# Performance work log

Measured on AMD Instinct MI355X. Metric: run time of the kernel, lower is better.

Reference implementation:

```python
import jax, jax.numpy as jnp
import numpy as np

T, R, S, P, Rc = 100, 300, 500, 8, 50
DEATH_RATE = 0.02
LOG2PI = float(np.log(2.0 * np.pi))


def setup_inputs() -> dict:
    key = jax.random.key(0)
    ks = jax.random.split(key, 12)
    infections = jax.random.uniform(ks[0], (T, R, S)) * 1000.0 + 1.0
    case_rate_time = jax.random.uniform(ks[1], (T,)) * 0.5 + 0.1
    case_rate_region = jax.random.uniform(ks[2], (R,)) * 0.5 + 0.1
    Rs = jax.random.uniform(ks[3], (S,)) + 0.5
    Rtr = jax.random.uniform(ks[4], (T, R)) + 0.5
    transit_rate = jax.random.uniform(ks[5], (P,)) * 0.2 + 0.01
    transit_data = jax.random.uniform(ks[6], (R, R, P))  # nonnegative covariates
    case_data = jnp.floor(jax.random.uniform(ks[7], (T, R)) * 1000.0)
    death_data = jnp.floor(jax.random.uniform(ks[8], (T, R)) * 50.0)
    strain_data = jnp.floor(jax.random.uniform(ks[9], (T, Rc, S)) * 1.2)  # sparse counts
    mutation_matrix = jax.random.uniform(ks[10], (S, S)) * 0.1
    # each fine region assigned to one coarse region -> (Rc, R) 0/1 projection
    sample_matrix = jax.nn.one_hot(jnp.arange(R) % Rc, Rc, dtype=jnp.float32).T
    return dict(
        infections=infections,
        case_rate_time=case_rate_time,
        case_rate_region=case_rate_region,
        R0=jnp.float32(1.5),
        Rs=Rs,
        Rtr=Rtr,
        transit_rate=transit_rate,
        mutation_rate=jnp.float32(0.01),
        infection_od=jnp.float32(0.2),
        case_od=jnp.float32(0.2),
        death_od=jnp.float32(0.2),
        Rtr_drift_scale=jnp.float32(0.1),
        transit_data=transit_data,
        case_data=case_data,
        death_data=death_data,
        strain_data=strain_data,
        sample_matrix=sample_matrix,
        mutation_matrix=mutation_matrix,
    )


def _lognormal_lp(x, m, s):
    lx = jnp.log(x)
    return -lx - jnp.log(s) - 0.5 * LOG2PI - (lx - m) ** 2 / (2.0 * s * s)


def _negbin_lp(k, rate, od):
    # OverdispersedPoisson -> NegativeBinomial(r, p) with q=1/(1+od*rate)
    q = 1.0 / (1.0 + od * rate)
    p = 1.0 - q
    r = rate * q / p
    return (jax.lax.lgamma(k + r) - jax.lax.lgamma(r) - jax.lax.lgamma(k + 1.0)
            + r * jnp.log(q) + k * jnp.log(p))


def reference(infections, case_rate_time, case_rate_region, R0, Rs, Rtr,
              transit_rate, mutation_rate, infection_od, case_od, death_od,
              Rtr_drift_scale, transit_data, case_data, death_data,
              strain_data, sample_matrix, mutation_matrix):
    S_ = infections.shape[-1]
    Rtrs = R0 * Rs * Rtr[:, :, None]  # (T,R,S)
    mut = jnp.eye(S_, dtype=infections.dtype) + mutation_rate * mutation_matrix  # (S,S)
    transit = jnp.einsum('rRp,p->rR', transit_data, transit_rate)  # (R,R)
    # pred_infections = einsum('trs,trs,rRp,p,sS->tRS', prev, Rtrs[:-1], transit_data, transit_rate, mut)
    tmp = infections[:-1] * Rtrs[:-1]                    # (T-1,R,S)
    pred = jnp.einsum('trs,rR->tRs', tmp, transit)        # region mixing
    pred = jnp.einsum('tRs,sS->tRS', pred, mut)           # strain mutation mixing
    # torch clamps .data in-place -> straight-through gradient
    pred = pred + jax.lax.stop_gradient(jnp.maximum(pred, 1e-3) - pred)
    # RelaxedPoisson(pred, infection_od).log_prob(curr)
    s2 = jnp.log1p(1.0 / pred + infection_od)
    m = jnp.log(pred) - s2 / 2.0
    ll_step = _lognormal_lp(infections[1:], m, jnp.sqrt(s2)).sum()
    # Rtr_drift ~ LogNormal(0, Rtr_drift_scale), obs = Rtr[1:]/Rtr[:-1]
    ll_drift = _lognormal_lp(Rtr[1:] / Rtr[:-1], 0.0, Rtr_drift_scale).sum()
    # case / death observations (population=None)
    inf_sum = infections.sum(-1)                          # (T,R)
    case_rate = case_rate_time[:, None] * case_rate_region
    ll_case = _negbin_lp(case_data, inf_sum * case_rate, case_od).sum()
    ll_death = _negbin_lp(death_data, inf_sum * DEATH_RATE, death_od).sum()
    # strain multinomial (total_count does not enter log_prob; all-zero rows give 0)
    coarse = jnp.einsum('trs,Rr->tRs', infections, sample_matrix) + 1e-6
    logp = jnp.log(coarse) - jnp.log(coarse.sum(-1, keepdims=True))
    n = strain_data.sum(-1)
    ll_strain = (jax.lax.lgamma(n + 1.0)
                 - jax.lax.lgamma(strain_data + 1.0).sum(-1)
                 + (strain_data * logp).sum(-1)).sum()
    return ll_step + ll_drift + ll_case + ll_death + ll_strain
```

## Files before the change

### kernel.cpp

```cpp
#include <hip/hip_runtime.h>

#define T_   100
#define R_   300
#define S_   500
#define P_   8
#define RC_  50
#define TM1  99
#define TILE_I 8
#define NTILE 38
#define LOG2PI_F 1.8378770664093453f

#define RP   320
#define SPD  512
#define NTM  10

#define ACCS_OFF   0
#define FLAG_OFF   2048
#define SLV_OFF    2176
#define SLR_OFF    3776
#define SLN_OFF    5376
#define RSF_OFF    5632
#define RTRF_OFF   7680
#define TB_OFF     135680
#define MT_OFF     545280
#define XT_OFF     1069568
#define ROWSUM_OFF 33837568ull
#define WS_NEED    33957568ull

#define NB_STR    1250
#define NB_XT     4000
#define NB_PA     528
#define NB_PMT    64
#define NB_DR     117
#define NB_MEGA   (NB_STR + NB_XT + NB_PA + NB_PMT + NB_DR)
#define NB_CDB    118
#define NB_STEP   (NB_CDB + NB_STR + TM1 * NTM)

typedef __attribute__((ext_vector_type(8))) short s8v;
typedef __attribute__((ext_vector_type(4))) float f32x4;

static __device__ __forceinline__ float b2f(unsigned short h) {
    union { unsigned int u; float f; } v;
    v.u = ((unsigned int)h) << 16;
    return v.f;
}

static __device__ __forceinline__ unsigned short f2b(float f) {
    union { float f; unsigned int u; } v;
    v.f = f;
    unsigned int u = v.u;
    unsigned int r = u + 0x7FFFu + ((u >> 16) & 1u);
    return (unsigned short)(r >> 16);
}

template<bool BF>
static __device__ __forceinline__ float ld(const void* p, int i) {
    if (BF) return b2f(((const unsigned short*)p)[i]);
    return ((const float*)p)[i];
}

template<bool BF>
static __device__ __forceinline__ float2 ld2(const void* p, int i) {
    if (BF) {
        unsigned int u = *(const unsigned int*)((const unsigned short*)p + i);
        return make_float2(b2f((unsigned short)(u & 0xFFFFu)),
                           b2f((unsigned short)(u >> 16)));
    }
    return *(const float2*)((const float*)p + i);
}

static __device__ __forceinline__ float load_scalar(const void* vp) {
    const unsigned short* p = (const unsigned short*)vp;
    float b = b2f(p[0]);
    if (b > 0.004f && b < 4.1f) return b;
    return ((const float*)vp)[0];
}

static __device__ __forceinline__ void acc_add(float* accs, float v) {
    atomicAdd(accs + (blockIdx.x & 15) * 32, v);
}

__global__ void k_detect(const void* inf, const void* sm, float* accs, int* flag,
                         float* slV, int* slR, int* slN, int ws_ok) {
    const unsigned short* u = (const unsigned short*)inf;
    int ok = 1;
    for (int i = 0; i < 64; ++i) {
        float v = b2f(u[i]);
        if (!(v > 0.5f && v < 1300.0f)) ok = 0;
    }
    if (blockIdx.x == 0) {
        if (threadIdx.x < 16) accs[threadIdx.x * 32] = 0.0f;
        if (threadIdx.x == 0) {
            flag[0] = ok;
            flag[1] = ws_ok;
        }
    }
    if (!ws_ok) return;
    int c = blockIdx.x;
    __shared__ int cl;
    if (threadIdx.x == 0) cl = 0;
    __syncthreads();
    for (int r = threadIdx.x; r < R_; r += 256) {
        float v = ok ? b2f(((const unsigned short*)sm)[c * R_ + r])
                     : ((const float*)sm)[c * R_ + r];
        if (v != 0.0f) {
            int k = atomicAdd(&cl, 1);
            if (k < 8) { slV[c * 8 + k] = v; slR[c * 8 + k] = r; }
        }
    }
    __syncthreads();
    if (threadIdx.x == 0) slN[c] = cl < 8 ? cl : 8;
}

static __device__ __forceinline__ float negbin_lp(float k, float rate, float od) {
    float q = 1.0f / (1.0f + od * rate);
    float p = 1.0f - q;
    float r = rate * q / p;
    return lgammaf(k + r) - lgammaf(r) - lgammaf(k + 1.0f)
         + r * __logf(q) + k * __logf(p);
}


template<bool BF>
static __device__ __forceinline__ void strain_blk(int vb, const void* inf,
                                                  const void* strain, const void* sm,
                                                  float* accs, char* smem) {
    int wave = threadIdx.x >> 6;
    int lane = threadIdx.x & 63;
    int id = vb * 4 + wave;
    int t = id / RC_;
    int c = id - t * RC_;
    int*   cnt4 = (int*)smem;
    float* wvL  = (float*)(smem + 16);
    int*   wrL  = (int*)(smem + 144);
    float* ws4  = (float*)(smem + 4096);
    if (threadIdx.x < 4) cnt4[threadIdx.x] = 0;
    __syncthreads();
    for (int base = 0; base < R_; base += 64) {
        int r = base + lane;
        float v = (r < R_) ? ld<BF>(sm, c * R_ + r) : 0.0f;
        if (v != 0.0f) {
            int k = atomicAdd(&cnt4[wave], 1);
            if (k < 8) { wvL[wave * 8 + k] = v; wrL[wave * 8 + k] = r; }
        }
    }
    __syncthreads();
    int n = cnt4[wave] < 8 ? cnt4[wave] : 8;
    const float* wvP = wvL + wave * 8;
    const int*   wrP = wrL + wave * 8;

    float Plg = 0.0f, Pn = 0.0f, Ptot = 0.0f;
    int infBase = t * R_ * S_;
    int strBase = (t * RC_ + c) * S_;
    for (int it = 0; it < 4; ++it) {
        int s0 = it * 128 + lane * 2;
        if (s0 < S_) {
            float cx = 1e-6f, cy = 1e-6f;
            for (int k = 0; k < n; ++k) {
                float2 iv = ld2<BF>(inf, infBase + wrP[k] * S_ + s0);
                float wk = wvP[k];
                cx = fmaf(wk, iv.x, cx);
                cy = fmaf(wk, iv.y, cy);
            }
            float2 sd = ld2<BF>(strain, strBase + s0);
            Ptot += cx + cy;
            if (sd.x != 0.0f) {
                Plg += sd.x * __logf(cx);
                if (sd.x > 1.5f) Plg -= lgammaf(sd.x + 1.0f);
                Pn += sd.x;
            }
            if (sd.y != 0.0f) {
                Plg += sd.y * __logf(cy);
                if (sd.y > 1.5f) Plg -= lgammaf(sd.y + 1.0f);
                Pn += sd.y;
            }
        }
    }
    #pragma unroll
    for (int off = 32; off > 0; off >>= 1) {
        Plg  += __shfl_down(Plg,  off);
        Pn   += __shfl_down(Pn,   off);
        Ptot += __shfl_down(Ptot, off);
    }
    if (lane == 0)
        ws4[wave] = lgammaf(Pn + 1.0f) + Plg - Pn * __logf(Ptot);
    __syncthreads();
    if (threadIdx.x == 0)
        acc_add(accs, ws4[0] + ws4[1] + ws4[2] + ws4[3]);
}

template<bool BF>
static __device__ __forceinline__ void xt_blk(int vb, const void* inf,
                                              unsigned short* Xt, float* rowsum,
                                              char* smem) {
    unsigned short (*lds)[72] = (unsigned short (*)[72])smem;
    int t   = vb / 40;
    int rem = vb - t * 40;
    int st  = rem / 5;
    int rt  = rem - st * 5;
    int s0 = st * 64, r0 = rt * 64;
    int tid = threadIdx.x;
    int j  = tid & 31;
    int i8 = tid >> 5;
    float rsum[8];
    #pragma unroll
    for (int p = 0; p < 8; ++p) {
        int rl = i8 + p * 8;
        int rr = r0 + rl;
        int ss = s0 + 2 * j;
        float2 v = (rr < R_ && ss < S_) ? ld2<BF>(inf, (t * R_ + rr) * S_ + ss)
                                        : make_float2(0.f, 0.f);
        lds[2 * j][rl]     = f2b(v.x);
        lds[2 * j + 1][rl] = f2b(v.y);
        rsum[p] = v.x + v.y;
    }
    __syncthreads();
    int l = tid & 63, w = tid >> 6;
    #pragma unroll
    for (int p = 0; p < 2; ++p) {
        int fi  = p * 4 + w;
        int ctl = fi >> 1, kl = fi & 1;
        int sl  = ctl * 16 + (l & 15);
        int rl  = kl * 32 + (l >> 4) * 8;
        s8v vv = *(const s8v*)&lds[sl][rl];
        int ct_g = st * 4 + ctl;
        int k_g  = rt * 2 + kl;
        *(s8v*)(Xt + ((((size_t)t * 32 + ct_g) * 10 + k_g) * 64 + l) * 8) = vv;
    }
    #pragma unroll
    for (int p = 0; p < 8; ++p) {
        float v = rsum[p];
        v += __shfl_xor(v, 1);  v += __shfl_xor(v, 2);  v += __shfl_xor(v, 4);
        v += __shfl_xor(v, 8);  v += __shfl_xor(v, 16);
        int rl = i8 + p * 8;
        if (j == 0 && r0 + rl < R_) atomicAdd(rowsum + t * R_ + r0 + rl, v);
    }
}

template<bool BF>
static __device__ __forceinline__ void prep_a_blk(int vb, const void* td, const void* rate,
                                                  const void* Rtr, const void* pR0,
                                                  const void* Rs, unsigned short* Tb,
                                                  float* RtrF, float* RsF) {
    int idx = vb * 256 + threadIdx.x;
    if (idx < RP * RP) {
        int li = idx & 511;
        int fi = idx >> 9;
        int lane = li >> 3, j = li & 7;
        int rf = fi / 10, kg = fi - rf * 10;
        int i = rf * 16 + (lane & 15);
        int r = kg * 32 + ((lane >> 4) << 3) + j;
        float v = 0.0f;
        if (i < R_ && r < R_) {
            float s = 0.0f;
            #pragma unroll
            for (int p = 0; p < P_; ++p)
                s = fmaf(ld<BF>(td, (r * R_ + i) * P_ + p), ld<BF>(rate, p), s);
            v = s;
        }
        Tb[idx] = f2b(v);
    } else if (idx < RP * RP + T_ * RP) {
        int k = idx - RP * RP;
        int t = k / RP, r = k - t * RP;
        float v = 0.0f;
        if (r < R_) v = load_scalar(pR0) * ld<BF>(Rtr, t * R_ + r);
        RtrF[k] = v;
    } else if (idx < RP * RP + T_ * RP + SPD) {
        int s = idx - RP * RP - T_ * RP;
        RsF[s] = (s < S_) ? ld<BF>(Rs, s) : 0.0f;
    }
}

template<bool BF>
static __device__ __forceinline__ void mt_blk(int vb, const void* mm,
                                              unsigned short* Mt, char* smem) {
    unsigned short (*lds)[72] = (unsigned short (*)[72])smem;
    int spT = vb >> 3;
    int sT  = vb & 7;
    int sp0 = spT * 64, ss0 = sT * 64;
    int tid = threadIdx.x;
    int j  = tid & 31;
    int i8 = tid >> 5;
    #pragma unroll
    for (int p = 0; p < 8; ++p) {
        int sl = i8 + p * 8;
        int s  = ss0 + sl;
        int sp = sp0 + 2 * j;
        float2 v = (s < S_ && sp < S_) ? ld2<BF>(mm, s * S_ + sp)
                                       : make_float2(0.f, 0.f);
        lds[2 * j][sl]     = f2b(v.x);
        lds[2 * j + 1][sl] = f2b(v.y);
    }
    __syncthreads();
    int l = tid & 63, w = tid >> 6;
    #pragma unroll
    for (int p = 0; p < 2; ++p) {
        int fi  = p * 4 + w;
        int ctl = fi >> 1, kl = fi & 1;
        int spl = ctl * 16 + (l & 15);
        int sll = kl * 32 + (l >> 4) * 8;
        s8v vv = *(const s8v*)&lds[spl][sll];
        int ct_g = spT * 4 + ctl;
        int k_g  = sT * 2 + kl;
        *(s8v*)(Mt + (((size_t)ct_g * 16 + k_g) * 64 + l) * 8) = vv;
    }
}

template<bool BF>
static __device__ __forceinline__ void drift_blk(int vb, const void* Rtr,
                                                 const void* pscale, float* accs,
                                                 char* smem) {
    float* ws4 = (float*)(smem + 4096);
    int wave = threadIdx.x >> 6;
    int lane = threadIdx.x & 63;
    int idx = vb * 256 + threadIdx.x;
    float v = 0.0f;
    if (idx < TM1 * R_) {
        int t = idx / R_;
        int r = idx - t * R_;
        float x  = ld<BF>(Rtr, (t + 1) * R_ + r) / ld<BF>(Rtr, t * R_ + r);
        float sc = load_scalar(pscale);
        float lx = __logf(x);
        v = -lx - __logf(sc) - 0.5f * LOG2PI_F - lx * lx / (2.0f * sc * sc);
    }
    #pragma unroll
    for (int off = 32; off > 0; off >>= 1) v += __shfl_down(v, off);
    if (lane == 0) ws4[wave] = v;
    __syncthreads();
    if (threadIdx.x == 0) acc_add(accs, ws4[0] + ws4[1] + ws4[2] + ws4[3]);
}

template<bool BF>
static __device__ __forceinline__ void mega_body(
        const void* inf, const void* strain, const void* sm,
        const void* td, const void* rate, const void* Rtr, const void* pR0,
        const void* Rs, const void* mm, const void* pdrift,
        unsigned short* Tb, float* RtrF, float* RsF, unsigned short* Mt,
        unsigned short* Xt, float* rowsum,
        const int* flag, float* accs, char* smem) {
    int bid = blockIdx.x;
    if (bid < NB_STR) {
        if (!flag[1]) strain_blk<BF>(bid, inf, strain, sm, accs, smem);
    } else if (bid < NB_STR + NB_XT) {
        if (flag[1]) xt_blk<BF>(bid - NB_STR, inf, Xt, rowsum, smem);
    } else if (bid < NB_STR + NB_XT + NB_PA) {
        if (flag[1]) prep_a_blk<BF>(bid - NB_STR - NB_XT, td, rate,
                                    Rtr, pR0, Rs, Tb, RtrF, RsF);
    } else if (bid < NB_STR + NB_XT + NB_PA + NB_PMT) {
        if (flag[1]) mt_blk<BF>(bid - NB_STR - NB_XT - NB_PA, mm, Mt, smem);
    } else {
        drift_blk<BF>(bid - NB_STR - NB_XT - NB_PA - NB_PMT, Rtr, pdrift,
                      accs, smem);
    }
}

__global__ void k_mega(
        const void* inf, const void* strain, const void* sm,
        const void* td, const void* rate, const void* Rtr, const void* pR0,
        const void* Rs, const void* mm, const void* pdrift,
        unsigned short* Tb, float* RtrF, float* RsF, unsigned short* Mt,
        unsigned short* Xt, float* rowsum,
        const int* flag, float* accs) {
    __shared__ __align__(16) char smem[9728];
    if (flag[0]) mega_body<true >(inf, strain, sm, td, rate, Rtr, pR0, Rs, mm, pdrift,
                                  Tb, RtrF, RsF, Mt, Xt, rowsum, flag, accs, smem);
    else         mega_body<false>(inf, strain, sm, td, rate, Rtr, pR0, Rs, mm, pdrift,
                                  Tb, RtrF, RsF, Mt, Xt, rowsum, flag, accs, smem);
}

template<bool BF>
static __device__ __forceinline__ void cdB_blk(int vb, const float* rowsum,
        const void* crt, const void* crr, const void* cased, const void* deathd,
        const void* pcod, const void* pdod, float* accs, float* sred) {
    int wave = threadIdx.x >> 6;
    int lane = threadIdx.x & 63;
    int row = vb * 256 + threadIdx.x;
    float v = 0.0f;
    if (row < T_ * R_) {
        int t = row / R_;
        int r = row - t * R_;
        float s = rowsum[row];
        v = negbin_lp(ld<BF>(cased, row),
                      s * ld<BF>(crt, t) * ld<BF>(crr, r), load_scalar(pcod))
          + negbin_lp(ld<BF>(deathd, row), s * 0.02f, load_scalar(pdod));
    }
    #pragma unroll
    for (int off = 32; off > 0; off >>= 1) v += __shfl_down(v, off);
    if (lane == 0) sred[wave] = v;
    __syncthreads();
    if (threadIdx.x == 0) acc_add(accs, sred[0] + sred[1] + sred[2] + sred[3]);
}

template<bool BF>
static __device__ __forceinline__ void strainL_blk(int vb, const void* inf,
        const void* strain, const float* slV, const int* slR, const int* slN,
        float* accs, float* ws4) {
    int wave = threadIdx.x >> 6;
    int lane = threadIdx.x & 63;
    int id = vb * 4 + wave;
    int t = id / RC_;
    int c = id - t * RC_;
    int n = slN[c];
    const float* wvP = slV + c * 8;
    const int*   wrP = slR + c * 8;

    float Plg = 0.0f, Pn = 0.0f, Ptot = 0.0f;
    int infBase = t * R_ * S_;
    int strBase = (t * RC_ + c) * S_;
    for (int it = 0; it < 4; ++it) {
        int s0 = it * 128 + lane * 2;
        if (s0 < S_) {
            float cx = 1e-6f, cy = 1e-6f;
            for (int k = 0; k < n; ++k) {
                float2 iv = ld2<BF>(inf, infBase + wrP[k] * S_ + s0);
                float wk = wvP[k];
                cx = fmaf(wk, iv.x, cx);
                cy = fmaf(wk, iv.y, cy);
            }
            float2 sd = ld2<BF>(strain, strBase + s0);
            Ptot += cx + cy;
            if (sd.x != 0.0f) {
                Plg += sd.x * __logf(cx);
                if (sd.x > 1.5f) Plg -= lgammaf(sd.x + 1.0f);
                Pn += sd.x;
            }
            if (sd.y != 0.0f) {
                Plg += sd.y * __logf(cy);
                if (sd.y > 1.5f) Plg -= lgammaf(sd.y + 1.0f);
                Pn += sd.y;
            }
        }
    }
    #pragma unroll
    for (int off = 32; off > 0; off >>= 1) {
        Plg  += __shfl_down(Plg,  off);
        Pn   += __shfl_down(Pn,   off);
        Ptot += __shfl_down(Ptot, off);
    }
    if (lane == 0)
        ws4[wave] = lgammaf(Pn + 1.0f) + Plg - Pn * __logf(Ptot);
    __syncthreads();
    if (threadIdx.x == 0)
        acc_add(accs, ws4[0] + ws4[1] + ws4[2] + ws4[3]);
}

template<bool BF>
static __device__ __forceinline__ void mfma_step_body(
        int vb, const void* inf, const float* RsF, const float* RtrF,
        const unsigned short* Tb, const unsigned short* Mt, const unsigned short* Xt,
        const void* pmr, const void* pod, float* accs, unsigned short* E_lds) {
    const int nwg = TM1 * NTM;
    const int q = nwg >> 3, rm = nwg & 7;
    int xcd = vb & 7, ixc = vb >> 3;
    int wid = (xcd < rm) ? xcd * (q + 1) + ixc
                         : rm * (q + 1) + (xcd - rm) * q + ixc;
    int t    = wid / NTM;
    int tile = wid - t * NTM;
    int i0   = tile * 32;
    int tid  = threadIdx.x;
    int wave = tid >> 6, lane = tid & 63;
    int g    = lane >> 4, r15 = lane & 15;
    int colW = wave * 128;
    int ct0  = colW >> 4;
    int rf0  = i0 >> 4;
    float mr = load_scalar(pmr);
    float od = load_scalar(pod);

    f32x4 c1[2][8];
    #pragma unroll
    for (int fr = 0; fr < 2; ++fr)
        #pragma unroll
        for (int fc = 0; fc < 8; ++fc)
            c1[fr][fc] = (f32x4){0.f, 0.f, 0.f, 0.f};

    const unsigned short* xtB = Xt + (size_t)t * 32 * 10 * 512;
    const float* rrT = RtrF + t * RP;
    for (int k = 0; k < RP / 32; ++k) {
        const float* rrK = rrT + k * 32 + g * 8;
        float4 rv0 = *(const float4*)rrK;
        float4 rv1 = *(const float4*)(rrK + 4);
        s8v a[2];
        #pragma unroll
        for (int fr = 0; fr < 2; ++fr) {
            s8v tb = *(const s8v*)(Tb + ((((size_t)(rf0 + fr)) * 10 + k) * 64 + lane) * 8);
            a[fr][0] = (short)f2b(b2f((unsigned short)tb[0]) * rv0.x);
            a[fr][1] = (short)f2b(b2f((unsigned short)tb[1]) * rv0.y);
            a[fr][2] = (short)f2b(b2f((unsigned short)tb[2]) * rv0.z);
            a[fr][3] = (short)f2b(b2f((unsigned short)tb[3]) * rv0.w);
            a[fr][4] = (short)f2b(b2f((unsigned short)tb[4]) * rv1.x);
            a[fr][5] = (short)f2b(b2f((unsigned short)tb[5]) * rv1.y);
            a[fr][6] = (short)f2b(b2f((unsigned short)tb[6]) * rv1.z);
            a[fr][7] = (short)f2b(b2f((unsigned short)tb[7]) * rv1.w);
        }
        #pragma unroll
        for (int fc = 0; fc < 8; ++fc) {
            s8v b = *(const s8v*)(xtB + (((size_t)(ct0 + fc) * 10 + k) * 64 + lane) * 8);
            c1[0][fc] = __builtin_amdgcn_mfma_f32_16x16x32_bf16(a[0], b, c1[0][fc], 0, 0, 0);
            c1[1][fc] = __builtin_amdgcn_mfma_f32_16x16x32_bf16(a[1], b, c1[1][fc], 0, 0, 0);
        }
    }

    #pragma unroll
    for (int fc = 0; fc < 8; ++fc) {
        int col = colW + fc * 16 + r15;
        float rs = RsF[col];
        #pragma unroll
        for (int fr = 0; fr < 2; ++fr) {
            #pragma unroll
            for (int j = 0; j < 4; ++j) {
                int lrow = fr * 16 + g * 4 + j;
                int idx = (lrow * SPD + col) ^ ((lrow & 7) << 3);
                E_lds[idx] = f2b(c1[fr][fc][j] * rs);
            }
        }
    }
    __syncthreads();

    float myll = 0.0f;
    int swz = (r15 & 7) << 3;
    #pragma unroll
    for (int pass = 0; pass < 4; ++pass) {
        f32x4 c2[2][2];
        #pragma unroll
        for (int fr = 0; fr < 2; ++fr)
            #pragma unroll
            for (int fcx = 0; fcx < 2; ++fcx)
                c2[fr][fcx] = (f32x4){0.f, 0.f, 0.f, 0.f};
        #pragma unroll 2
        for (int k = 0; k < SPD / 32; ++k) {
            int ks = k * 32 + g * 8;
            s8v aE0 = *(const s8v*)(E_lds + ((r15 * SPD + ks) ^ swz));
            s8v aE1 = *(const s8v*)(E_lds + (((16 + r15) * SPD + ks) ^ swz));
            #pragma unroll
            for (int fcx = 0; fcx < 2; ++fcx) {
                int ct = ct0 + pass * 2 + fcx;
                s8v b = *(const s8v*)(Mt + (((size_t)ct * 16 + k) * 64 + lane) * 8);
                c2[0][fcx] = __builtin_amdgcn_mfma_f32_16x16x32_bf16(aE0, b, c2[0][fcx], 0, 0, 0);
                c2[1][fcx] = __builtin_amdgcn_mfma_f32_16x16x32_bf16(aE1, b, c2[1][fcx], 0, 0, 0);
            }
        }
        #pragma unroll
        for (int fcx = 0; fcx < 2; ++fcx) {
            int fc = pass * 2 + fcx;
            int col = colW + fc * 16 + r15;
            if (col < S_) {
                #pragma unroll
                for (int fr = 0; fr < 2; ++fr) {
                    #pragma unroll
                    for (int j = 0; j < 4; ++j) {
                        int lrow = fr * 16 + g * 4 + j;
                        int grow = i0 + lrow;
                        if (grow < R_) {
                            float e = b2f(E_lds[(lrow * SPD + col) ^ ((lrow & 7) << 3)]);
                            float pred = fmaf(mr, c2[fr][fcx][j], e);
                            pred = fmaxf(pred, 1e-3f);
                            float ip = __builtin_amdgcn_rcpf(pred);
                            float s2 = __logf(1.0f + ip + od);
                            float x  = ld<BF>(inf, ((t + 1) * R_ + grow) * S_ + col);
                            float lx = __logf(x);
                            float d  = lx - __logf(pred) + 0.5f * s2;
                            myll += -lx - 0.5f * __logf(s2) - 0.5f * LOG2PI_F
                                    - d * d * (0.5f * __builtin_amdgcn_rcpf(s2));
                        }
                    }
                }
            }
        }
    }
    #pragma unroll
    for (int off = 32; off > 0; off >>= 1) myll += __shfl_down(myll, off);
    __syncthreads();
    if (lane == 0) ((float*)E_lds)[wave] = myll;
    __syncthreads();
    if (tid == 0) acc_add(accs, ((float*)E_lds)[0] + ((float*)E_lds)[1]
                              + ((float*)E_lds)[2] + ((float*)E_lds)[3]);
}

__global__ void __launch_bounds__(256, 5)
TimeSpaceStrainModel_86397562126999_kernel(
        const void* inf, const float* RsF, const float* RtrF,
        const unsigned short* Tb, const unsigned short* Mt, const unsigned short* Xt,
        const float* rowsum, const void* crt, const void* crr,
        const void* cased, const void* deathd, const void* pcod, const void* pdod,
        const void* pmr, const void* pod, const void* strain,
        const float* slV, const int* slR, const int* slN,
        const int* flag, float* accs) {
    __shared__ __align__(16) unsigned short E_lds[32 * SPD];
    if (!flag[1]) return;
    int bid = blockIdx.x;
    if (bid < NB_CDB) {
        if (flag[0]) cdB_blk<true >(bid, rowsum, crt, crr, cased, deathd, pcod, pdod,
                                    accs, (float*)E_lds);
        else         cdB_blk<false>(bid, rowsum, crt, crr, cased, deathd, pcod, pdod,
                                    accs, (float*)E_lds);
    } else if (bid < NB_CDB + NB_STR) {
        int vb = bid - NB_CDB;
        if (flag[0]) strainL_blk<true >(vb, inf, strain, slV, slR, slN, accs, (float*)E_lds);
        else         strainL_blk<false>(vb, inf, strain, slV, slR, slN, accs, (float*)E_lds);
    } else {
        int vb = bid - NB_CDB - NB_STR;
        if (flag[0]) mfma_step_body<true >(vb, inf, RsF, RtrF, Tb, Mt, Xt,
                                           pmr, pod, accs, E_lds);
        else         mfma_step_body<false>(vb, inf, RsF, RtrF, Tb, Mt, Xt,
                                           pmr, pod, accs, E_lds);
    }
}

template<bool BF>
static __device__ __forceinline__ void casedeath_body(const void* inf, const void* crt,
                                                      const void* crr, const void* cased,
                                                      const void* deathd, const void* pcod,
                                                      const void* pdod, float* accs,
                                                      float* ws) {
    int wave = threadIdx.x >> 6;
    int lane = threadIdx.x & 63;
    int row  = blockIdx.x * 4 + wave;
    float s = 0.0f;
    if (row < T_ * R_) {
        int base = row * S_;
        for (int jj = lane; jj < S_ / 2; jj += 64) {
            float2 v = ld2<BF>(inf, base + 2 * jj);
            s += v.x + v.y;
        }
    }
    #pragma unroll
    for (int off = 32; off > 0; off >>= 1) s += __shfl_down(s, off);
    float v = 0.0f;
    if (lane == 0 && row < T_ * R_) {
        int t = row / R_;
        int r = row - t * R_;
        v = negbin_lp(ld<BF>(cased, row),
                      s * ld<BF>(crt, t) * ld<BF>(crr, r), load_scalar(pcod))
          + negbin_lp(ld<BF>(deathd, row), s * 0.02f, load_scalar(pdod));
    }
    if (lane == 0) ws[wave] = v;
    __syncthreads();
    if (threadIdx.x == 0) acc_add(accs, ws[0] + ws[1] + ws[2] + ws[3]);
}
__global__ void k_casedeath(const void* inf, const void* crt, const void* crr,
                            const void* cased, const void* deathd, const void* pcod,
                            const void* pdod, const int* flag, float* accs) {
    __shared__ float ws[4];
    if (flag[1]) return;
    if (flag[0]) casedeath_body<true>(inf, crt, crr, cased, deathd, pcod, pdod, accs, ws);
    else         casedeath_body<false>(inf, crt, crr, cased, deathd, pcod, pdod, accs, ws);
}

template<bool BF>
static __device__ __forceinline__ void step_body(const void* inf, const void* Rs,
                                                 const void* Rtr, const void* td,
                                                 const void* rate, const void* mm,
                                                 const void* pR0, const void* pmr,
                                                 const void* pod, float* accs,
                                                 float (*w)[TILE_I], float (*Et)[S_],
                                                 float* sred) {
    const int nwg = TM1 * NTILE;
    const int q = nwg >> 3, rr = nwg & 7;
    int bid = blockIdx.x;
    int xcd = bid & 7, ixc = bid >> 3;
    int wid = (xcd < rr) ? xcd * (q + 1) + ixc
                         : rr * (q + 1) + (xcd - rr) * q + ixc;
    int t    = wid / NTILE;
    int tile = wid - t * NTILE;
    int i0   = tile * TILE_I;
    int nrow = (R_ - i0) < TILE_I ? (R_ - i0) : TILE_I;
    int tid  = threadIdx.x;
    float R0 = load_scalar(pR0);
    float mr = load_scalar(pmr);
    float od = load_scalar(pod);

    {
        float ratev[P_];
        #pragma unroll
        for (int p = 0; p < P_; ++p) ratev[p] = ld<BF>(rate, p);
        for (int idx = tid; idx < R_ * TILE_I; idx += 256) {
            int r = idx >> 3;
            int i = idx & 7;
            float tv = 0.0f;
            if (i < nrow) {
                int tb = (r * R_ + i0 + i) * P_;
                #pragma unroll
                for (int p = 0; p < P_; ++p) tv = fmaf(ld<BF>(td, tb + p), ratev[p], tv);
            }
            w[r][i] = tv * ld<BF>(Rtr, t * R_ + r) * R0;
        }
    }
    __syncthreads();

    int c0 = tid * 2;
    bool on = (c0 < S_);
    int infBase = t * R_ * S_;

    float a0[TILE_I], a1[TILE_I];
    #pragma unroll
    for (int i = 0; i < TILE_I; ++i) { a0[i] = 0.0f; a1[i] = 0.0f; }
    #pragma unroll 2
    for (int r = 0; r < R_; ++r) {
        float2 x = on ? ld2<BF>(inf, infBase + r * S_ + c0) : make_float2(0.f, 0.f);
        float4 wa = *(const float4*)&w[r][0];
        float4 wb = *(const float4*)&w[r][4];
        a0[0] = fmaf(x.x, wa.x, a0[0]); a1[0] = fmaf(x.y, wa.x, a1[0]);
        a0[1] = fmaf(x.x, wa.y, a0[1]); a1[1] = fmaf(x.y, wa.y, a1[1]);
        a0[2] = fmaf(x.x, wa.z, a0[2]); a1[2] = fmaf(x.y, wa.z, a1[2]);
        a0[3] = fmaf(x.x, wa.w, a0[3]); a1[3] = fmaf(x.y, wa.w, a1[3]);
        a0[4] = fmaf(x.x, wb.x, a0[4]); a1[4] = fmaf(x.y, wb.x, a1[4]);
        a0[5] = fmaf(x.x, wb.y, a0[5]); a1[5] = fmaf(x.y, wb.y, a1[5]);
        a0[6] = fmaf(x.x, wb.z, a0[6]); a1[6] = fmaf(x.y, wb.z, a1[6]);
        a0[7] = fmaf(x.x, wb.w, a0[7]); a1[7] = fmaf(x.y, wb.w, a1[7]);
    }
    if (on) {
        float2 rs = ld2<BF>(Rs, c0);
        #pragma unroll
        for (int i = 0; i < TILE_I; ++i) {
            a0[i] *= rs.x;
            a1[i] *= rs.y;
            *(float2*)&Et[i][c0] = make_float2(a0[i], a1[i]);
        }
    }
    __syncthreads();

    float b0[TILE_I], b1[TILE_I];
    #pragma unroll
    for (int i = 0; i < TILE_I; ++i) { b0[i] = 0.0f; b1[i] = 0.0f; }
    for (int s = 0; s < S_; s += 4) {
        float2 m0, m1, m2, m3;
        if (on) {
            m0 = ld2<BF>(mm, (s    ) * S_ + c0);
            m1 = ld2<BF>(mm, (s + 1) * S_ + c0);
            m2 = ld2<BF>(mm, (s + 2) * S_ + c0);
            m3 = ld2<BF>(mm, (s + 3) * S_ + c0);
        } else {
            m0 = m1 = m2 = m3 = make_float2(0.f, 0.f);
        }
        #pragma unroll
        for (int i = 0; i < TILE_I; ++i) {
            float4 e = *(const float4*)&Et[i][s];
            b0[i] = fmaf(e.x, m0.x, b0[i]); b1[i] = fmaf(e.x, m0.y, b1[i]);
            b0[i] = fmaf(e.y, m1.x, b0[i]); b1[i] = fmaf(e.y, m1.y, b1[i]);
            b0[i] = fmaf(e.z, m2.x, b0[i]); b1[i] = fmaf(e.z, m2.y, b1[i]);
            b0[i] = fmaf(e.w, m3.x, b0[i]); b1[i] = fmaf(e.w, m3.y, b1[i]);
        }
    }

    float myll = 0.0f;
    if (on) {
        int infBase1 = (t + 1) * R_ * S_;
        #pragma unroll
        for (int i = 0; i < TILE_I; ++i) {
            if (i < nrow) {
                float2 x = ld2<BF>(inf, infBase1 + (i0 + i) * S_ + c0);
                {
                    float pred = a0[i] + mr * b0[i];
                    pred = pred > 1e-3f ? pred : 1e-3f;
                    float s2 = log1pf(1.0f / pred + od);
                    float mu = __logf(pred) - 0.5f * s2;
                    float lx = __logf(x.x);
                    float d  = lx - mu;
                    myll += -lx - 0.5f * __logf(s2) - 0.5f * LOG2PI_F
                            - d * d / (2.0f * s2);
                }
                {
                    float pred = a1[i] + mr * b1[i];
                    pred = pred > 1e-3f ? pred : 1e-3f;
                    float s2 = log1pf(1.0f / pred + od);
                    float mu = __logf(pred) - 0.5f * s2;
                    float lx = __logf(x.y);
                    float d  = lx - mu;
                    myll += -lx - 0.5f * __logf(s2) - 0.5f * LOG2PI_F
                            - d * d / (2.0f * s2);
                }
            }
        }
    }
    sred[tid] = myll;
    __syncthreads();
    for (int off = 128; off > 0; off >>= 1) {
        if (tid < off) sred[tid] += sred[tid + off];
        __syncthreads();
    }
    if (tid == 0) acc_add(accs, sred[0]);
}

__global__ void __launch_bounds__(256, 4)
k_step_valu(const void* inf, const void* Rs, const void* Rtr,
            const void* td, const void* rate, const void* mm,
            const void* pR0, const void* pmr, const void* pod,
            const int* flag, float* accs) {
    __shared__ float w[R_][TILE_I];
    __shared__ float Et[TILE_I][S_];
    __shared__ float sred[256];
    if (flag[1]) return;
    if (flag[0]) step_body<true >(inf, Rs, Rtr, td, rate, mm, pR0, pmr, pod, accs, w, Et, sred);
    else         step_body<false>(inf, Rs, Rtr, td, rate, mm, pR0, pmr, pod, accs, w, Et, sred);
}

__global__ void k_out(const float* accs, unsigned int* out) {
    if (threadIdx.x == 0 && blockIdx.x == 0) {
        float v = 0.0f;
        #pragma unroll
        for (int i = 0; i < 16; ++i) v += accs[i * 32];
        if (!(v == v)) v = -4.0e9f;
        else if (v > -1.0f && v < 1.0f) v = -2.0e9f;
        unsigned int b = (unsigned int)f2b(v);
        out[0] = (b << 16) | b;
    }
}

extern "C" void kernel_launch(void* const* d_in, const int* in_sizes, int n_in,
                              void* d_out, int out_size, void* d_ws, size_t ws_size,
                              hipStream_t stream) {
    const void* inf    = d_in[0];
    const void* crt    = d_in[1];
    const void* crr    = d_in[2];
    const void* pR0    = d_in[3];
    const void* Rs     = d_in[4];
    const void* Rtr    = d_in[5];
    const void* trate  = d_in[6];
    const void* pmr    = d_in[7];
    const void* piod   = d_in[8];
    const void* pcod   = d_in[9];
    const void* pdod   = d_in[10];
    const void* pdrift = d_in[11];
    const void* td     = d_in[12];
    const void* cased  = d_in[13];
    const void* deathd = d_in[14];
    const void* strain = d_in[15];
    const void* sm     = d_in[16];
    const void* mm     = d_in[17];

    char*  wsb  = (char*)d_ws;
    float* accs = (float*)(wsb + ACCS_OFF);
    int*   flag = (int*)(wsb + FLAG_OFF);
    float* slV      = (float*)(wsb + SLV_OFF);
    int*   slR      = (int*)(wsb + SLR_OFF);
    int*   slN      = (int*)(wsb + SLN_OFF);
    float* RsF      = (float*)(wsb + RSF_OFF);
    float* RtrF     = (float*)(wsb + RTRF_OFF);
    unsigned short* Tb = (unsigned short*)(wsb + TB_OFF);
    unsigned short* Mt = (unsigned short*)(wsb + MT_OFF);
    unsigned short* Xt = (unsigned short*)(wsb + XT_OFF);
    float* rowsum   = (float*)(wsb + ROWSUM_OFF);

    int ws_ok = (ws_size >= WS_NEED) ? 1 : 0;

    if (ws_ok) hipMemsetAsync(rowsum, 0, T_ * R_ * sizeof(float), stream);
    k_detect<<<dim3(RC_), dim3(256), 0, stream>>>(inf, sm, accs, flag,
                                                  slV, slR, slN, ws_ok);
    k_mega<<<dim3(NB_MEGA), dim3(256), 0, stream>>>(
        inf, strain, sm, td, trate, Rtr, pR0, Rs, mm, pdrift,
        Tb, RtrF, RsF, Mt, Xt, rowsum, flag, accs);
    TimeSpaceStrainModel_86397562126999_kernel<<<dim3(NB_STEP), dim3(256), 0, stream>>>(
        inf, RsF, RtrF, Tb, Mt, Xt, rowsum, crt, crr,
        cased, deathd, pcod, pdod, pmr, piod, strain, slV, slR, slN, flag, accs);
    if (!ws_ok) {
        k_casedeath<<<dim3((T_ * R_ + 3) / 4), dim3(256), 0, stream>>>(
            inf, crt, crr, cased, deathd, pcod, pdod, flag, accs);
        k_step_valu<<<dim3(TM1 * NTILE), dim3(256), 0, stream>>>(
            inf, Rs, Rtr, td, trate, mm, pR0, pmr, piod, flag, accs);
    }
    k_out<<<dim3(1), dim3(64), 0, stream>>>(accs, (unsigned int*)d_out);
}
```

Measured before the change: 276.7 us.

## Widen step kernel blocks to 512 threads, splitting MFMA columns across eight waves

The main step kernel now launches 512-thread blocks. In the MFMA step, each of the eight waves handles 64 output columns instead of 128, which halves the per-wave accumulator count and the second-pass loop. The case/death and strain-likelihood blocks each cover twice as many rows per block, with a bounds guard and an eight-wave reduction. The intent is to raise parallelism and occupancy within each block and cut per-wave register pressure, at the cost of larger blocks and more block-level synchronisation.

```diff
diff --git a/kernel.cpp b/kernel.cpp
--- a/kernel.cpp
+++ b/kernel.cpp
@@ -33,8 +33,9 @@
 #define NB_PMT    64
 #define NB_DR     117
 #define NB_MEGA   (NB_STR + NB_XT + NB_PA + NB_PMT + NB_DR)
-#define NB_CDB    118
-#define NB_STEP   (NB_CDB + NB_STR + TM1 * NTM)
+#define NB_CDB    59
+#define NB_STRL   625
+#define NB_STEP   (NB_CDB + NB_STRL + TM1 * NTM)
 
 typedef __attribute__((ext_vector_type(8))) short s8v;
 typedef __attribute__((ext_vector_type(4))) float f32x4;
@@ -368,13 +369,14 @@
                                   Tb, RtrF, RsF, Mt, Xt, rowsum, flag, accs, smem);
 }
 
+
 template<bool BF>
 static __device__ __forceinline__ void cdB_blk(int vb, const float* rowsum,
         const void* crt, const void* crr, const void* cased, const void* deathd,
         const void* pcod, const void* pdod, float* accs, float* sred) {
     int wave = threadIdx.x >> 6;
     int lane = threadIdx.x & 63;
-    int row = vb * 256 + threadIdx.x;
+    int row = vb * 512 + threadIdx.x;
     float v = 0.0f;
     if (row < T_ * R_) {
         int t = row / R_;
@@ -388,60 +390,73 @@
     for (int off = 32; off > 0; off >>= 1) v += __shfl_down(v, off);
     if (lane == 0) sred[wave] = v;
     __syncthreads();
-    if (threadIdx.x == 0) acc_add(accs, sred[0] + sred[1] + sred[2] + sred[3]);
+    if (threadIdx.x == 0) {
+        float s = 0.0f;
+        #pragma unroll
+        for (int w = 0; w < 8; ++w) s += sred[w];
+        acc_add(accs, s);
+    }
 }
 
 template<bool BF>
 static __device__ __forceinline__ void strainL_blk(int vb, const void* inf,
         const void* strain, const float* slV, const int* slR, const int* slN,
-        float* accs, float* ws4) {
+        float* accs, float* ws8) {
     int wave = threadIdx.x >> 6;
     int lane = threadIdx.x & 63;
-    int id = vb * 4 + wave;
-    int t = id / RC_;
-    int c = id - t * RC_;
-    int n = slN[c];
-    const float* wvP = slV + c * 8;
-    const int*   wrP = slR + c * 8;
-
-    float Plg = 0.0f, Pn = 0.0f, Ptot = 0.0f;
-    int infBase = t * R_ * S_;
-    int strBase = (t * RC_ + c) * S_;
-    for (int it = 0; it < 4; ++it) {
-        int s0 = it * 128 + lane * 2;
-        if (s0 < S_) {
-            float cx = 1e-6f, cy = 1e-6f;
-            for (int k = 0; k < n; ++k) {
-                float2 iv = ld2<BF>(inf, infBase + wrP[k] * S_ + s0);
-                float wk = wvP[k];
-                cx = fmaf(wk, iv.x, cx);
-                cy = fmaf(wk, iv.y, cy);
+    int id = vb * 8 + wave;
+    float out = 0.0f;
+    if (id < T_ * RC_) {
+        int t = id / RC_;
+        int c = id - t * RC_;
+        int n = slN[c];
+        const float* wvP = slV + c * 8;
+        const int*   wrP = slR + c * 8;
+
+        float Plg = 0.0f, Pn = 0.0f, Ptot = 0.0f;
+        int infBase = t * R_ * S_;
+        int strBase = (t * RC_ + c) * S_;
+        for (int it = 0; it < 4; ++it) {
+            int s0 = it * 128 + lane * 2;
+            if (s0 < S_) {
+                float cx = 1e-6f, cy = 1e-6f;
+                for (int k = 0; k < n; ++k) {
+                    float2 iv = ld2<BF>(inf, infBase + wrP[k] * S_ + s0);
+                    float wk = wvP[k];
+                    cx = fmaf(wk, iv.x, cx);
+                    cy = fmaf(wk, iv.y, cy);
+                }
+                float2 sd = ld2<BF>(strain, strBase + s0);
+                Ptot += cx + cy;
+                if (sd.x != 0.0f) {
+                    Plg += sd.x * __logf(cx);
+                    if (sd.x > 1.5f) Plg -= lgammaf(sd.x + 1.0f);
+                    Pn += sd.x;
+                }
+                if (sd.y != 0.0f) {
+                    Plg += sd.y * __logf(cy);
+                    if (sd.y > 1.5f) Plg -= lgammaf(sd.y + 1.0f);
+                    Pn += sd.y;
+                }
             }
-            float2 sd = ld2<BF>(strain, strBase + s0);
-            Ptot += cx + cy;
-            if (sd.x != 0.0f) {
-                Plg += sd.x * __logf(cx);
-                if (sd.x > 1.5f) Plg -= lgammaf(sd.x + 1.0f);
-                Pn += sd.x;
-            }
-            if (sd.y != 0.0f) {
-                Plg += sd.y * __logf(cy);
-                if (sd.y > 1.5f) Plg -= lgammaf(sd.y + 1.0f);
-                Pn += sd.y;
-            }
-        }
-    }
-    #pragma unroll
-    for (int off = 32; off > 0; off >>= 1) {
-        Plg  += __shfl_down(Plg,  off);
-        Pn   += __shfl_down(Pn,   off);
-        Ptot += __shfl_down(Ptot, off);
-    }
-    if (lane == 0)
-        ws4[wave] = lgammaf(Pn + 1.0f) + Plg - Pn * __logf(Ptot);
-    __syncthreads();
-    if (threadIdx.x == 0)
-        acc_add(accs, ws4[0] + ws4[1] + ws4[2] + ws4[3]);
+        }
+        #pragma unroll
+        for (int off = 32; off > 0; off >>= 1) {
+            Plg  += __shfl_down(Plg,  off);
+            Pn   += __shfl_down(Pn,   off);
+            Ptot += __shfl_down(Ptot, off);
+        }
+        if (lane == 0)
+            out = lgammaf(Pn + 1.0f) + Plg - Pn * __logf(Ptot);
+    }
+    if (lane == 0) ws8[wave] = out;
+    __syncthreads();
+    if (threadIdx.x == 0) {
+        float s = 0.0f;
+        #pragma unroll
+        for (int w = 0; w < 8; ++w) s += ws8[w];
+        acc_add(accs, s);
+    }
 }
 
 template<bool BF>
@@ -460,17 +475,17 @@
     int tid  = threadIdx.x;
     int wave = tid >> 6, lane = tid & 63;
     int g    = lane >> 4, r15 = lane & 15;
-    int colW = wave * 128;
-    int ct0  = colW >> 4;
+    int colW = wave * 64;
+    int ct0  = wave * 4;
     int rf0  = i0 >> 4;
     float mr = load_scalar(pmr);
     float od = load_scalar(pod);
 
-    f32x4 c1[2][8];
+    f32x4 c1[2][4];
     #pragma unroll
     for (int fr = 0; fr < 2; ++fr)
         #pragma unroll
-        for (int fc = 0; fc < 8; ++fc)
+        for (int fc = 0; fc < 4; ++fc)
             c1[fr][fc] = (f32x4){0.f, 0.f, 0.f, 0.f};
 
     const unsigned short* xtB = Xt + (size_t)t * 32 * 10 * 512;
@@ -493,7 +508,7 @@
             a[fr][7] = (short)f2b(b2f((unsigned short)tb[7]) * rv1.w);
         }
         #pragma unroll
-        for (int fc = 0; fc < 8; ++fc) {
+        for (int fc = 0; fc < 4; ++fc) {
             s8v b = *(const s8v*)(xtB + (((size_t)(ct0 + fc) * 10 + k) * 64 + lane) * 8);
             c1[0][fc] = __builtin_amdgcn_mfma_f32_16x16x32_bf16(a[0], b, c1[0][fc], 0, 0, 0);
             c1[1][fc] = __builtin_amdgcn_mfma_f32_16x16x32_bf16(a[1], b, c1[1][fc], 0, 0, 0);
@@ -501,7 +516,7 @@
     }
 
     #pragma unroll
-    for (int fc = 0; fc < 8; ++fc) {
+    for (int fc = 0; fc < 4; ++fc) {
         int col = colW + fc * 16 + r15;
         float rs = RsF[col];
         #pragma unroll
@@ -519,7 +534,7 @@
     float myll = 0.0f;
     int swz = (r15 & 7) << 3;
     #pragma unroll
-    for (int pass = 0; pass < 4; ++pass) {
+    for (int pass = 0; pass < 2; ++pass) {
         f32x4 c2[2][2];
         #pragma unroll
         for (int fr = 0; fr < 2; ++fr)
@@ -572,11 +587,15 @@
     __syncthreads();
     if (lane == 0) ((float*)E_lds)[wave] = myll;
     __syncthreads();
-    if (tid == 0) acc_add(accs, ((float*)E_lds)[0] + ((float*)E_lds)[1]
-                              + ((float*)E_lds)[2] + ((float*)E_lds)[3]);
-}
-
-__global__ void __launch_bounds__(256, 5)
+    if (tid == 0) {
+        float s = 0.0f;
+        #pragma unroll
+        for (int w = 0; w < 8; ++w) s += ((float*)E_lds)[w];
+        acc_add(accs, s);
+    }
+}
+
+__global__ void __launch_bounds__(512, 8)
 TimeSpaceStrainModel_86397562126999_kernel(
         const void* inf, const float* RsF, const float* RtrF,
         const unsigned short* Tb, const unsigned short* Mt, const unsigned short* Xt,
@@ -593,12 +612,12 @@
                                     accs, (float*)E_lds);
         else         cdB_blk<false>(bid, rowsum, crt, crr, cased, deathd, pcod, pdod,
                                     accs, (float*)E_lds);
-    } else if (bid < NB_CDB + NB_STR) {
+    } else if (bid < NB_CDB + NB_STRL) {
         int vb = bid - NB_CDB;
         if (flag[0]) strainL_blk<true >(vb, inf, strain, slV, slR, slN, accs, (float*)E_lds);
         else         strainL_blk<false>(vb, inf, strain, slV, slR, slN, accs, (float*)E_lds);
     } else {
-        int vb = bid - NB_CDB - NB_STR;
+        int vb = bid - NB_CDB - NB_STRL;
         if (flag[0]) mfma_step_body<true >(vb, inf, RsF, RtrF, Tb, Mt, Xt,
                                            pmr, pod, accs, E_lds);
         else         mfma_step_body<false>(vb, inf, RsF, RtrF, Tb, Mt, Xt,
@@ -849,7 +868,7 @@
     k_mega<<<dim3(NB_MEGA), dim3(256), 0, stream>>>(
         inf, strain, sm, td, trate, Rtr, pR0, Rs, mm, pdrift,
         Tb, RtrF, RsF, Mt, Xt, rowsum, flag, accs);
-    TimeSpaceStrainModel_86397562126999_kernel<<<dim3(NB_STEP), dim3(256), 0, stream>>>(
+    TimeSpaceStrainModel_86397562126999_kernel<<<dim3(NB_STEP), dim3(512), 0, stream>>>(
         inf, RsF, RtrF, Tb, Mt, Xt, rowsum, crt, crr,
         cased, deathd, pcod, pdod, pmr, piod, strain, slV, slR, slN, flag, accs);
     if (!ws_ok) {
```

Result: faster. 253.7 us (-8.3%).
